# Kernel optimization log

Measured on AMD Instinct MI355X. Metric: run time of the kernel, lower is better.

The kernel has to match this reference:

```python
import jax, jax.numpy as jnp
import numpy as np

B, D, E, H, O, K = 8192, 3072, 8, 2048, 512, 2
EPS = float(np.finfo(float).eps)  # np.finfo(float).eps used in SparseDispatcher.combine


def _cv_squared(v):
    # torch .var() is unbiased (ddof=1)
    v = v.astype(jnp.float32)
    return jnp.var(v, ddof=1) / (jnp.mean(v) ** 2 + 1e-10)


def setup_inputs() -> dict:
    key = jax.random.key(0)
    ks = jax.random.split(key, 8)
    x = jax.random.normal(ks[0], (B, D), dtype=jnp.float32)
    Cats = jax.random.uniform(ks[1], (B, E), dtype=jnp.float32)
    w_gate = jax.random.normal(ks[2], (D, E), dtype=jnp.float32) * 0.01
    # per-expert 2-layer MLP standing in for the per-expert ResNet
    W1 = jax.random.normal(ks[3], (E, D, H), dtype=jnp.float32) * (1.0 / np.sqrt(D))
    b1 = jnp.zeros((E, H), dtype=jnp.float32)
    W2 = jax.random.normal(ks[4], (E, H, O), dtype=jnp.float32) * (1.0 / np.sqrt(H))
    b2 = jnp.zeros((E, O), dtype=jnp.float32)
    return {"x": x, "Cats": Cats, "w_gate": w_gate, "W1": W1, "b1": b1,
            "W2": W2, "b2": b2, "train": 0}


def reference(x, Cats, w_gate, W1, b1, W2, b2, train):
    # ---- top_k_gating (eval path; train branch mutates optimizer state) ----
    logits = x @ w_gate                                   # [B, E]
    top_vals, top_idx = jax.lax.top_k(logits, min(K + 1, E))
    top_k_vals = top_vals[:, :K]                          # [B, K]
    top_k_idx = top_idx[:, :K]                            # [B, K]
    top_k_gates = jax.nn.softmax(top_k_vals, axis=1)      # softmax over kept logits
    rows = jnp.arange(x.shape[0])[:, None]
    gates = jnp.zeros_like(logits).at[rows, top_k_idx].set(top_k_gates)  # scatter

    load = (gates > 0).sum(axis=0)                        # tokens per expert
    importance = gates.sum(axis=0)
    aux_loss = 0.01 * (_cv_squared(importance) + _cv_squared(load))

    # ---- dispatch / expert / combine ----
    # Dense grouped form: expert_i runs on its routed tokens; tokens with
    # gates[b,i]==0 contribute exactly 0 to the combine, identical math to
    # SparseDispatcher's gather/split + exp*gate + index_add + log.
    h = jax.nn.relu(jnp.einsum('bd,edh->beh', x, W1) + b1[None])  # [B, E, H]
    out = jnp.einsum('beh,eho->beo', h, W2) + b2[None]            # [B, E, O]
    combined = jnp.einsum('be,beo->bo', gates, jnp.exp(out))      # exp, *gate, sum
    combined = jnp.where(combined == 0, EPS, combined)
    y = jnp.log(combined)
    return (y, aux_loss)
```

## Files before the change

### kernel.cpp

```cpp
#include <hip/hip_runtime.h>
#include <stdint.h>


typedef __bf16 bf16x8 __attribute__((ext_vector_type(8)));
typedef __bf16 bf16x4 __attribute__((ext_vector_type(4)));
typedef float floatx4 __attribute__((ext_vector_type(4)));

#define EPSF 2.2204460492503131e-16f

__device__ __forceinline__ void gl_lds16(const void* g, void* l) {
  __builtin_amdgcn_global_load_lds(
      (__attribute__((address_space(1))) void*)(g),
      (__attribute__((address_space(3))) void*)(l), 16, 0, 0);
}

__global__ __launch_bounds__(256) void k_gating(
    const float* __restrict__ x, const float* __restrict__ wg,
    __bf16* __restrict__ x_bf, int* __restrict__ expsel,
    float* __restrict__ gpair) {
  const int lane = threadIdx.x & 63;
  const int w = threadIdx.x >> 6;
  const int r = blockIdx.x * 4 + w;
  const float* xr = x + (size_t)r * 3072;
  __bf16* xbr = x_bf + (size_t)r * 3072;
  double acc[8];
#pragma unroll
  for (int e = 0; e < 8; ++e) acc[e] = 0.0;
  for (int t = 0; t < 12; ++t) {
    const int d = t * 256 + lane * 4;
    const float4 xv = *(const float4*)(xr + d);
    bf16x4 xo;
    xo.x = (__bf16)xv.x; xo.y = (__bf16)xv.y;
    xo.z = (__bf16)xv.z; xo.w = (__bf16)xv.w;
    *(bf16x4*)(xbr + d) = xo;
    const float* wrow = wg + (size_t)d * 8;
#pragma unroll
    for (int u = 0; u < 4; ++u) {
      const float xf = ((const float*)&xv)[u];
#pragma unroll
      for (int e = 0; e < 8; ++e)
        acc[e] += (double)xf * (double)wrow[u * 8 + e];
    }
  }
#pragma unroll
  for (int e = 0; e < 8; ++e) {
    double v = acc[e];
    v += __shfl_down(v, 32);
    v += __shfl_down(v, 16);
    v += __shfl_down(v, 8);
    v += __shfl_down(v, 4);
    v += __shfl_down(v, 2);
    v += __shfl_down(v, 1);
    acc[e] = v;
  }
  if (lane == 0) {
    int i0 = 0; double v0 = acc[0];
#pragma unroll
    for (int e = 1; e < 8; ++e) if (acc[e] > v0) { v0 = acc[e]; i0 = e; }
    int i1 = (i0 == 0) ? 1 : 0; double v1 = acc[i1];
#pragma unroll
    for (int e = 0; e < 8; ++e)
      if (e != i0 && acc[e] > v1 && e != i1) { v1 = acc[e]; i1 = e; }
    const float tt = (float)exp(v1 - v0);
    const float g0 = 1.0f / (1.0f + tt);
    const float g1 = tt / (1.0f + tt);
    expsel[r] = i0 | (i1 << 4);
    gpair[r * 2] = g0;
    gpair[r * 2 + 1] = g1;
  }
}

__global__ __launch_bounds__(256) void k_build_lists(
    const int* __restrict__ expsel, const float* __restrict__ gpair,
    int* __restrict__ lists, int* __restrict__ cnt, double* __restrict__ imp) {
  const int e = blockIdx.x;
  const int tid = threadIdx.x;
  const int lane = tid & 63;
  const int w = tid >> 6;
  __shared__ int wsum[4];
  __shared__ double dsum[4];
  int base = 0;
  double gsum = 0.0;
  int* out = lists + e * 8192;
  for (int c = 0; c < 32; ++c) {
    const int r = c * 256 + tid;
    const int sel = expsel[r];
    const bool m0 = ((sel & 15) == e);
    const bool m1 = (((sel >> 4) & 15) == e);
    const bool m = m0 || m1;
    const int entry = 2 * r + (m1 ? 1 : 0);
    const unsigned long long mask = __ballot(m);
    const int wcount = __popcll(mask);
    const int pos = __popcll(mask & ((1ull << lane) - 1ull));
    if (lane == 0) wsum[w] = wcount;
    __syncthreads();
    int pre = base;
#pragma unroll
    for (int ww = 0; ww < 4; ++ww) if (ww < w) pre += wsum[ww];
    const int total = wsum[0] + wsum[1] + wsum[2] + wsum[3];
    if (m) {
      out[pre + pos] = entry;
      gsum += (double)gpair[entry];
    }
    base += total;
    __syncthreads();
  }
  gsum += __shfl_down(gsum, 32);
  gsum += __shfl_down(gsum, 16);
  gsum += __shfl_down(gsum, 8);
  gsum += __shfl_down(gsum, 4);
  gsum += __shfl_down(gsum, 2);
  gsum += __shfl_down(gsum, 1);
  if (lane == 0) dsum[w] = gsum;
  __syncthreads();
  if (tid == 0) {
    imp[e] = dsum[0] + dsum[1] + dsum[2] + dsum[3];
    cnt[e] = base;
  }
}

__global__ void k_sched_aux(const int* __restrict__ cnt, const double* __restrict__ imp,
                            int* __restrict__ sched, int* __restrict__ nslots,
                            float* __restrict__ aux_out) {
  if (threadIdx.x != 0 || blockIdx.x != 0) return;
  int ns = 0;
  for (int e = 0; e < 8; ++e) {
    const int c = cnt[e];
    const int t = (c + 127) >> 7;
    for (int i = 0; i < t; ++i) { sched[2 * ns] = e; sched[2 * ns + 1] = i << 7; ++ns; }
  }
  *nslots = ns;
  double mi = 0.0, ml = 0.0;
  for (int e = 0; e < 8; ++e) { mi += imp[e]; ml += (double)cnt[e]; }
  mi *= 0.125; ml *= 0.125;
  double vi = 0.0, vl = 0.0;
  for (int e = 0; e < 8; ++e) {
    const double di = imp[e] - mi; vi += di * di;
    const double dl = (double)cnt[e] - ml; vl += dl * dl;
  }
  vi /= 7.0; vl /= 7.0;
  aux_out[0] = (float)(0.01 * (vi / (mi * mi + 1e-10) + vl / (ml * ml + 1e-10)));
}

__global__ __launch_bounds__(256) void k_transpose_cvt(
    const float* __restrict__ in, __bf16* __restrict__ out, int R, int C) {
  __shared__ float tile[64][65];
  const int e = blockIdx.z;
  const int c0 = blockIdx.x * 64;
  const int r0 = blockIdx.y * 64;
  const float* src = in + (size_t)e * R * C + (size_t)r0 * C + c0;
  __bf16* dst = out + (size_t)e * R * C + (size_t)c0 * R + r0;
  const int tx = threadIdx.x & 15;
  const int ty = threadIdx.x >> 4;
#pragma unroll
  for (int i = 0; i < 4; ++i) {
    const int row = ty + i * 16;
    const float4 v = *(const float4*)(src + (size_t)row * C + tx * 4);
    tile[row][tx * 4 + 0] = v.x;
    tile[row][tx * 4 + 1] = v.y;
    tile[row][tx * 4 + 2] = v.z;
    tile[row][tx * 4 + 3] = v.w;
  }
  __syncthreads();
#pragma unroll
  for (int i = 0; i < 4; ++i) {
    const int cc = ty + i * 16;
    const int rr = tx * 4;
    bf16x4 o;
    o.x = (__bf16)tile[rr + 0][cc];
    o.y = (__bf16)tile[rr + 1][cc];
    o.z = (__bf16)tile[rr + 2][cc];
    o.w = (__bf16)tile[rr + 3][cc];
    *(bf16x4*)(dst + (size_t)cc * R + rr) = o;
  }
}

template <int KDIM, int MODE>
__global__ __launch_bounds__(256, 2) void k_moe_gemm(
    const __bf16* __restrict__ Asrc, const __bf16* __restrict__ Ball,
    const float* __restrict__ bias, const int* __restrict__ lists,
    const int* __restrict__ cnt, const int* __restrict__ sched,
    const int* __restrict__ nslots, const float* __restrict__ gpair,
    __bf16* __restrict__ hout, float* __restrict__ oout) {
  constexpr int NDIM = (MODE == 0) ? 2048 : 512;
  const int slot = blockIdx.y;
  if (slot >= *nslots) return;
  const int e = sched[2 * slot];
  const int row0 = sched[2 * slot + 1];
  const int cnte = cnt[e];
  const int n0 = blockIdx.x * 128;

  __shared__ unsigned short As[128 * 32];
  __shared__ unsigned short Bs[128 * 32];

  const int tid = threadIdx.x;
  const int lane = tid & 63;
  const int wid = __builtin_amdgcn_readfirstlane(tid >> 6);
  const int wm = wid >> 1;
  const int wn = wid & 1;

  const __bf16* Be = Ball + (size_t)e * NDIM * KDIM;
  const int* liste = lists + e * 8192;
  const int acol = (lane & 3) * 8;

  const __bf16* aptr[2];
  const __bf16* bptr[2];
#pragma unroll
  for (int p = 0; p < 2; ++p) {
    const int chunk = wid + 4 * p;
    const int lr = chunk * 16 + (lane >> 2);
    int m = row0 + lr;
    m = (m < cnte) ? m : (cnte - 1);
    const int entry = liste[m];
    const int srow = (MODE == 0) ? (entry >> 1) : entry;
    aptr[p] = Asrc + (size_t)srow * KDIM + acol;
    bptr[p] = Be + (size_t)(n0 + lr) * KDIM + acol;
  }

  floatx4 acc[4][4];
#pragma unroll
  for (int i = 0; i < 4; ++i)
#pragma unroll
    for (int j = 0; j < 4; ++j) {
      acc[i][j].x = 0.f; acc[i][j].y = 0.f; acc[i][j].z = 0.f; acc[i][j].w = 0.f;
    }

  for (int k0 = 0; k0 < KDIM; k0 += 32) {
#pragma unroll
    for (int p = 0; p < 2; ++p) {
      gl_lds16(aptr[p] + k0, &As[(wid + 4 * p) * 512]);
      gl_lds16(bptr[p] + k0, &Bs[(wid + 4 * p) * 512]);
    }
    __syncthreads();
    bf16x8 af[4], bfr[4];
    const int rdoff = (lane & 15) * 32 + (lane >> 4) * 8;
#pragma unroll
    for (int i = 0; i < 4; ++i)
      af[i] = *(const bf16x8*)&As[(wm * 64 + i * 16) * 32 + rdoff];
#pragma unroll
    for (int j = 0; j < 4; ++j)
      bfr[j] = *(const bf16x8*)&Bs[(wn * 64 + j * 16) * 32 + rdoff];
    __syncthreads();
#pragma unroll
    for (int i = 0; i < 4; ++i)
#pragma unroll
      for (int j = 0; j < 4; ++j)
        acc[i][j] = __builtin_amdgcn_mfma_f32_16x16x32_bf16(af[i], bfr[j], acc[i][j], 0, 0, 0);
  }

  const int cq = lane >> 4;
  const int cn = lane & 15;
#pragma unroll
  for (int i = 0; i < 4; ++i) {
#pragma unroll
    for (int r = 0; r < 4; ++r) {
      const int m = row0 + wm * 64 + i * 16 + cq * 4 + r;
      if (m < cnte) {
        const int p = liste[m];
        if (MODE == 0) {
          __bf16* orow = hout + (size_t)p * 2048;
#pragma unroll
          for (int j = 0; j < 4; ++j) {
            const int n = n0 + wn * 64 + j * 16 + cn;
            float v = acc[i][j][r] + bias[e * 2048 + n];
            v = v > 0.0f ? v : 0.0f;
            orow[n] = (__bf16)v;
          }
        } else {
          float* orow = oout + (size_t)p * 512;
          const float g = gpair[p];
#pragma unroll
          for (int j = 0; j < 4; ++j) {
            const int n = n0 + wn * 64 + j * 16 + cn;
            const float v = acc[i][j][r] + bias[e * 512 + n];
            orow[n] = g * __expf(v);
          }
        }
      }
    }
  }
}

__global__ __launch_bounds__(128) void k_combine(const float* __restrict__ op,
                                                 float* __restrict__ y) {
  const int r = blockIdx.x;
  const int o = threadIdx.x * 4;
  const float4 a = *(const float4*)(op + (size_t)(2 * r) * 512 + o);
  const float4 b = *(const float4*)(op + (size_t)(2 * r + 1) * 512 + o);
  float4 res;
  float s;
  s = a.x + b.x; if (s == 0.0f) s = EPSF; res.x = logf(s);
  s = a.y + b.y; if (s == 0.0f) s = EPSF; res.y = logf(s);
  s = a.z + b.z; if (s == 0.0f) s = EPSF; res.z = logf(s);
  s = a.w + b.w; if (s == 0.0f) s = EPSF; res.w = logf(s);
  *(float4*)(y + (size_t)r * 512 + o) = res;
}

extern "C" void kernel_launch(void* const* d_in, const int* in_sizes, int n_in,
                              void* d_out, int out_size, void* d_ws, size_t ws_size,
                              hipStream_t stream) {
  (void)in_sizes; (void)n_in; (void)out_size; (void)ws_size;
  const float* x  = (const float*)d_in[0];
  const float* wg = (const float*)d_in[2];
  const float* W1 = (const float*)d_in[3];
  const float* b1 = (const float*)d_in[4];
  const float* W2 = (const float*)d_in[5];
  const float* b2 = (const float*)d_in[6];
  float* y = (float*)d_out;

  char* w = (char*)d_ws;
  __bf16* x_bf = (__bf16*)w; w += (size_t)8192 * 3072 * 2;
  __bf16* w1t  = (__bf16*)w; w += (size_t)8 * 2048 * 3072 * 2;
  __bf16* w2t  = (__bf16*)w; w += (size_t)8 * 512 * 2048 * 2;
  __bf16* hp   = (__bf16*)w; w += (size_t)16384 * 2048 * 2;
  float*  op   = (float*)w;  w += (size_t)16384 * 512 * 4;
  int*    lists= (int*)w;    w += (size_t)8 * 8192 * 4;
  float*  gpr  = (float*)w;  w += (size_t)16384 * 4;
  int*    expsel=(int*)w;    w += (size_t)8192 * 4;
  int*    cnt  = (int*)w;    w += 64;
  double* imp  = (double*)w; w += 64;
  int*    sched= (int*)w;    w += 2 * 136 * 4;
  int*    nslots=(int*)w;    w += 64;

  hipLaunchKernelGGL(k_gating, dim3(2048), dim3(256), 0, stream, x, wg, x_bf, expsel, gpr);
  hipLaunchKernelGGL(k_build_lists, dim3(8), dim3(256), 0, stream, expsel, gpr, lists, cnt, imp);
  hipLaunchKernelGGL(k_transpose_cvt, dim3(32, 48, 8), dim3(256), 0, stream, W1, w1t, 3072, 2048);
  hipLaunchKernelGGL(k_transpose_cvt, dim3(8, 32, 8), dim3(256), 0, stream, W2, w2t, 2048, 512);
  hipLaunchKernelGGL(k_sched_aux, dim3(1), dim3(64), 0, stream, cnt, imp, sched, nslots,
                     y + (size_t)8192 * 512);
  hipLaunchKernelGGL((k_moe_gemm<3072, 0>), dim3(16, 136), dim3(256), 0, stream,
                     x_bf, w1t, b1, lists, cnt, sched, nslots, (const float*)nullptr,
                     hp, (float*)nullptr);
  hipLaunchKernelGGL((k_moe_gemm<2048, 1>), dim3(4, 136), dim3(256), 0, stream,
                     hp, w2t, b2, lists, cnt, sched, nslots, gpr,
                     (__bf16*)nullptr, op);
  hipLaunchKernelGGL(k_combine, dim3(8192), dim3(128), 0, stream, op, y);
}
```

Before: 856.5 us.

## Stage gate weights in LDS and split gating dot products across lanes per expert

The gating kernel now runs 8 rows per 512-thread block and stages w_gate halves into padded shared memory. Each lane computes one expert's partial dot product over a 192-element slice with two double accumulators, and results are reduced with xor shuffles instead of 8 separate 6-step reductions. This is meant to cut redundant global loads of the gate weights and the shuffle overhead of the fp64 per-lane 8-expert accumulation. The trade-offs are a second read of each x row, extra block barriers, and roughly 48KB of LDS per block, which may limit occupancy.

New measurement: 804.3 us. 6.1% less time.

```diff
diff --git a/kernel.cpp b/kernel.cpp
--- a/kernel.cpp
+++ b/kernel.cpp
@@ -14,18 +14,21 @@
       (__attribute__((address_space(3))) void*)(l), 16, 0, 0);
 }
 
-__global__ __launch_bounds__(256) void k_gating(
+__global__ __launch_bounds__(512) void k_gating(
     const float* __restrict__ x, const float* __restrict__ wg,
     __bf16* __restrict__ x_bf, int* __restrict__ expsel,
     float* __restrict__ gpair) {
-  const int lane = threadIdx.x & 63;
-  const int w = threadIdx.x >> 6;
-  const int r = blockIdx.x * 4 + w;
+  __shared__ float wgs[12320];
+  const int tid = threadIdx.x;
+  const int lane = tid & 63;
+  const int w = tid >> 6;
+  const int r = blockIdx.x * 8 + w;
+  const int g = lane >> 3;
+  const int e = lane & 7;
   const float* xr = x + (size_t)r * 3072;
   __bf16* xbr = x_bf + (size_t)r * 3072;
-  double acc[8];
-#pragma unroll
-  for (int e = 0; e < 8; ++e) acc[e] = 0.0;
+
+#pragma unroll
   for (int t = 0; t < 12; ++t) {
     const int d = t * 256 + lane * 4;
     const float4 xv = *(const float4*)(xr + d);
@@ -33,34 +36,44 @@
     xo.x = (__bf16)xv.x; xo.y = (__bf16)xv.y;
     xo.z = (__bf16)xv.z; xo.w = (__bf16)xv.w;
     *(bf16x4*)(xbr + d) = xo;
-    const float* wrow = wg + (size_t)d * 8;
-#pragma unroll
-    for (int u = 0; u < 4; ++u) {
-      const float xf = ((const float*)&xv)[u];
-#pragma unroll
-      for (int e = 0; e < 8; ++e)
-        acc[e] += (double)xf * (double)wrow[u * 8 + e];
-    }
-  }
-#pragma unroll
-  for (int e = 0; e < 8; ++e) {
-    double v = acc[e];
-    v += __shfl_down(v, 32);
-    v += __shfl_down(v, 16);
-    v += __shfl_down(v, 8);
-    v += __shfl_down(v, 4);
-    v += __shfl_down(v, 2);
-    v += __shfl_down(v, 1);
-    acc[e] = v;
-  }
+  }
+
+  double a0 = 0.0, a1 = 0.0;
+  for (int h = 0; h < 2; ++h) {
+    __syncthreads();
+#pragma unroll
+    for (int t = 0; t < 6; ++t) {
+      const int wi = t * 2048 + tid * 4;
+      const int gg = wi / 1536;
+      const float4 v = *(const float4*)(wg + h * 12288 + wi);
+      *(float4*)(wgs + wi + 4 * gg) = v;
+    }
+    __syncthreads();
+    const float* xrg = xr + h * 1536 + g * 192;
+    const float* wbase = wgs + g * 1540 + e;
+    for (int i = 0; i < 192; i += 4) {
+      const float4 xv = *(const float4*)(xrg + i);
+      a0 += (double)xv.x * (double)wbase[(i + 0) * 8];
+      a1 += (double)xv.y * (double)wbase[(i + 1) * 8];
+      a0 += (double)xv.z * (double)wbase[(i + 2) * 8];
+      a1 += (double)xv.w * (double)wbase[(i + 3) * 8];
+    }
+  }
+  double v = a0 + a1;
+  v += __shfl_xor(v, 8);
+  v += __shfl_xor(v, 16);
+  v += __shfl_xor(v, 32);
+  double le[8];
+#pragma unroll
+  for (int ee = 0; ee < 8; ++ee) le[ee] = __shfl(v, ee);
   if (lane == 0) {
-    int i0 = 0; double v0 = acc[0];
-#pragma unroll
-    for (int e = 1; e < 8; ++e) if (acc[e] > v0) { v0 = acc[e]; i0 = e; }
-    int i1 = (i0 == 0) ? 1 : 0; double v1 = acc[i1];
-#pragma unroll
-    for (int e = 0; e < 8; ++e)
-      if (e != i0 && acc[e] > v1 && e != i1) { v1 = acc[e]; i1 = e; }
+    int i0 = 0; double v0 = le[0];
+#pragma unroll
+    for (int k = 1; k < 8; ++k) if (le[k] > v0) { v0 = le[k]; i0 = k; }
+    int i1 = (i0 == 0) ? 1 : 0; double v1 = le[i1];
+#pragma unroll
+    for (int k = 0; k < 8; ++k)
+      if (k != i0 && le[k] > v1 && k != i1) { v1 = le[k]; i1 = k; }
     const float tt = (float)exp(v1 - v0);
     const float g0 = 1.0f / (1.0f + tt);
     const float g1 = tt / (1.0f + tt);
@@ -322,7 +335,7 @@
   int*    sched= (int*)w;    w += 2 * 136 * 4;
   int*    nslots=(int*)w;    w += 64;
 
-  hipLaunchKernelGGL(k_gating, dim3(2048), dim3(256), 0, stream, x, wg, x_bf, expsel, gpr);
+  hipLaunchKernelGGL(k_gating, dim3(1024), dim3(512), 0, stream, x, wg, x_bf, expsel, gpr);
   hipLaunchKernelGGL(k_build_lists, dim3(8), dim3(256), 0, stream, expsel, gpr, lists, cnt, imp);
   hipLaunchKernelGGL(k_transpose_cvt, dim3(32, 48, 8), dim3(256), 0, stream, W1, w1t, 3072, 2048);
   hipLaunchKernelGGL(k_transpose_cvt, dim3(8, 32, 8), dim3(256), 0, stream, W2, w2t, 2048, 512);
```
